# Kernel optimization log

Hardware: AMD Instinct MI355X
Metric: run time of the kernel (lower is better)

The kernel has to match this reference:

```python
import jax, jax.numpy as jnp
import numpy as np

N_ELEM = 10   # len(EnvPara.ELEMENTS)
N_ATOMS = 100000
N_DIM = 256


def setup_inputs() -> dict:
    key = jax.random.key(0)
    k = jax.random.split(key, 5)
    return {
        "input_tensor": jax.random.normal(k[0], (N_ATOMS, N_DIM), jnp.float32),
        "species": jax.random.randint(k[1], (N_ATOMS,), 0, N_ELEM, dtype=jnp.int64),
        "W1": jax.random.normal(k[2], (N_ELEM, N_DIM, N_DIM), jnp.float32) / np.sqrt(N_DIM).astype(np.float32),
        "b1": jnp.zeros((N_ELEM, N_DIM), jnp.float32),
        "W2": jax.random.normal(k[3], (N_ELEM, N_DIM, 1), jnp.float32) / np.sqrt(N_DIM).astype(np.float32),
        "b2": jnp.zeros((N_ELEM, 1), jnp.float32),
    }


def _element_linear(x, species, W, b):
    # Species-routed linear: each atom uses the weight/bias of its element.
    # Loop over the small fixed element set (N_ELEM=10) to avoid materializing
    # a [n_atoms, d_in, d_out] gathered-weight tensor.
    out = jnp.zeros((x.shape[0], W.shape[2]), dtype=x.dtype)
    for e in range(W.shape[0]):
        mask = (species == e)[:, None]                      # [n_atoms, 1]
        out = out + jnp.where(mask, x @ W[e] + b[e], jnp.zeros((), x.dtype))
    return out


def reference(input_tensor, species, W1, b1, W2, b2):
    # layer2(silu(layer1(x)))
    h = _element_linear(input_tensor, species, W1, b1)      # [n_atoms, n_dim]
    h = jax.nn.silu(h)                                      # way=0 -> plain SiLU
    return _element_linear(h, species, W2, b2)              # [n_atoms, 1]
```

## Files before the change

kernel.cpp:

```cpp
#include <hip/hip_runtime.h>
#include <hip/hip_bf16.h>
#include <stdint.h>


#define NDIM 256
#define CHUNKS 16
#define BCHUNK 16384
#define TROWS 32
#define ROWB 1040
#define MAXT 16
#define NB_GEMM 256

typedef __attribute__((ext_vector_type(8))) short short8;
typedef __attribute__((ext_vector_type(8))) unsigned short ushort8;
typedef __attribute__((ext_vector_type(4))) float f32x4;

__device__ __forceinline__ unsigned short f2bf(float f) {
  unsigned u = __float_as_uint(f);
  u = (u + 0x7FFFu + ((u >> 16) & 1u)) >> 16;
  return (unsigned short)u;
}

__device__ __forceinline__ void gload_lds16(const void* gsrc, void* ldst) {
  __builtin_amdgcn_global_load_lds(
      (const __attribute__((address_space(1))) unsigned*)gsrc,
      (__attribute__((address_space(3))) unsigned*)(uintptr_t)(unsigned)(uintptr_t)ldst,
      16, 0, 0);
}

__device__ __forceinline__ short8 cvt8(float4 lo, float4 hi) {
  union { short8 s; unsigned u[4]; } r;
  __hip_bfloat162 t;
  t = __float22bfloat162_rn(make_float2(lo.x, lo.y)); r.u[0] = *(unsigned*)&t;
  t = __float22bfloat162_rn(make_float2(lo.z, lo.w)); r.u[1] = *(unsigned*)&t;
  t = __float22bfloat162_rn(make_float2(hi.x, hi.y)); r.u[2] = *(unsigned*)&t;
  t = __float22bfloat162_rn(make_float2(hi.z, hi.w)); r.u[3] = *(unsigned*)&t;
  return r.s;
}


__global__ void convw_k(const float* __restrict__ W1, unsigned short* __restrict__ wt, int NE) {
  int t = blockIdx.x * 256 + threadIdx.x;
  if (t >= NE * 8192) return;
  int n = t & 255;
  int g = (t >> 8) & 3;
  int step = (t >> 10) & 7;
  int e = t >> 13;
  int k0 = step * 32 + g * 8;
  const float* src = W1 + ((size_t)e << 16) + (size_t)k0 * NDIM + n;
  unsigned short v[8];
  #pragma unroll
  for (int j = 0; j < 8; ++j) v[j] = f2bf(src[j * NDIM]);
  char* chunk = (char*)wt + (size_t)(e * 8 + step) * BCHUNK;
  unsigned off = ((unsigned)(n * 64 + g * 16)) ^ ((unsigned)((n & 7) << 4));
  *(ushort8*)(chunk + off) = *(ushort8*)v;
}

__global__ void bhist_k(const int* __restrict__ sp, int n, int* __restrict__ bc, int NE) {
  __shared__ int wc[4][16];
  int tid = threadIdx.x;
  int i = blockIdx.x * 256 + tid;
  int s = (i < n) ? sp[i] : -1;
  int w = tid >> 6, lane = tid & 63;
  for (int e = 0; e < NE; ++e) {
    unsigned long long m = __ballot(s == e);
    if (lane == 0) wc[w][e] = __popcll(m);
  }
  __syncthreads();
  if (tid < NE) bc[blockIdx.x * NE + tid] = wc[0][tid] + wc[1][tid] + wc[2][tid] + wc[3][tid];
}

__global__ void scan_k(const int* __restrict__ bc, int* __restrict__ bo,
                       int* __restrict__ atom_start, int* __restrict__ tile_off,
                       int* __restrict__ bstart, int nblocks, int NE) {
  __shared__ int csum[256];
  __shared__ int coff[256];
  __shared__ int stot[16];
  __shared__ int sbase[16];
  int tid = threadIdx.x;
  int per = (nblocks + CHUNKS - 1) / CHUNKS;
  int e = tid / CHUNKS, c = tid % CHUNKS;
  int b0 = c * per, b1 = b0 + per; if (b1 > nblocks) b1 = nblocks;
  if (tid < NE * CHUNKS) {
    int s = 0;
    for (int b = b0; b < b1; ++b) s += bc[b * NE + e];
    csum[tid] = s;
  }
  __syncthreads();
  if (tid < NE) {
    int r = 0;
    for (int c2 = 0; c2 < CHUNKS; ++c2) { coff[tid * CHUNKS + c2] = r; r += csum[tid * CHUNKS + c2]; }
    stot[tid] = r;
  }
  __syncthreads();
  if (tid == 0) {
    int a = 0, t = 0;
    for (int e2 = 0; e2 < NE; ++e2) {
      sbase[e2] = a;
      atom_start[e2] = a; tile_off[e2] = t;
      a += stot[e2]; t += (stot[e2] + TROWS - 1) / TROWS;
    }
    atom_start[NE] = a; tile_off[NE] = t;
    int ntl = t > 0 ? t : 1;
    int nbk[16]; int tot = 0, emax = 0;
    for (int e2 = 0; e2 < NE; ++e2) {
      int nt = tile_off[e2 + 1] - tile_off[e2];
      int v = (nt > 0) ? (int)(((long long)nt * NB_GEMM) / ntl) : 0;
      if (nt > 0 && v < 1) v = 1;
      nbk[e2] = v; tot += v;
      if (nbk[e2] > nbk[emax]) emax = e2;
    }
    nbk[emax] += NB_GEMM - tot;
    int bacc = 0;
    for (int e2 = 0; e2 < NE; ++e2) { bstart[e2] = bacc; bacc += nbk[e2]; }
    bstart[NE] = bacc;
  }
  __syncthreads();
  if (tid < NE * CHUNKS) {
    int run = sbase[e] + coff[tid];
    for (int b = b0; b < b1; ++b) { bo[b * NE + e] = run; run += bc[b * NE + e]; }
  }
}

__global__ void dscatter_k(const int* __restrict__ sp, int n, const int* __restrict__ bo,
                           int* __restrict__ sorted, int NE) {
  __shared__ int wc[4][16];
  int tid = threadIdx.x;
  int i = blockIdx.x * 256 + tid;
  int s = (i < n) ? sp[i] : -1;
  int w = tid >> 6, lane = tid & 63;
  for (int e = 0; e < NE; ++e) {
    unsigned long long m = __ballot(s == e);
    if (lane == 0) wc[w][e] = __popcll(m);
  }
  __syncthreads();
  for (int e = 0; e < NE; ++e) {
    unsigned long long m = __ballot(s == e);
    if (s == e) {
      int wpre = 0;
      for (int w2 = 0; w2 < 4; ++w2) if (w2 < w) wpre += wc[w2][e];
      int rank = __popcll(m & ((1ull << lane) - 1ull));
      sorted[bo[blockIdx.x * NE + e] + wpre + rank] = i;
    }
  }
}


__global__ __launch_bounds__(512, 1) void gemm_k(
    const float* __restrict__ x, const unsigned short* __restrict__ wt,
    const float* __restrict__ b1, const float* __restrict__ w2,
    const float* __restrict__ b2, const int* __restrict__ sorted,
    const int* __restrict__ atom_start, const int* __restrict__ tile_off,
    const int* __restrict__ bstart, float* __restrict__ out, int NE)
{
  __shared__ __align__(16) char ldsA[3][TROWS * ROWB];
  __shared__ float partLds[256];
  __shared__ int ldsAtoms[MAXT * TROWS];
  __shared__ int toffs[17], astart[17], bst[17];

  int tid = threadIdx.x, lane = tid & 63, wid = tid >> 6;
  int lr = lane & 15, lg = lane >> 4;

  if (tid <= NE) {
    toffs[tid] = tile_off[tid]; astart[tid] = atom_start[tid]; bst[tid] = bstart[tid];
  }
  __syncthreads();

  int b = blockIdx.x;
  int e = 0;
  while (b >= bst[e + 1]) ++e;
  int j = b - bst[e], nbe = bst[e + 1] - bst[e];
  int nte = toffs[e + 1] - toffs[e];
  int q = nte / nbe, r = nte % nbe;
  int cnt = q + (j < r ? 1 : 0);
  if (cnt <= 0) return;
  int t0 = toffs[e] + j * q + (j < r ? j : r);
  int t1 = t0 + cnt;

  {
    int rs0 = astart[e] + (t0 - toffs[e]) * TROWS;
    int rvAll = astart[e + 1] - rs0;
    for (int i = tid; i < cnt * TROWS; i += 512) {
      int rloc = (i < rvAll) ? i : (rvAll - 1);
      ldsAtoms[i] = sorted[rs0 + rloc];
    }
  }
  __syncthreads();

  short8 bf[2][8];
  float bbv[2], wvv[2];
  {
    const char* wbase = (const char*)wt + (size_t)e * 8 * BCHUNK;
    #pragma unroll
    for (int nf = 0; nf < 2; ++nf) {
      int ncol = wid * 32 + nf * 16 + lr;
      unsigned off = ((unsigned)(ncol * 64 + lg * 16)) ^ ((unsigned)((ncol & 7) << 4));
      #pragma unroll
      for (int s = 0; s < 8; ++s)
        bf[nf][s] = *(const short8*)(wbase + (size_t)s * BCHUNK + off);
      bbv[nf] = b1[(size_t)e * NDIM + ncol];
      wvv[nf] = w2[(size_t)e * NDIM + ncol];
    }
  }
  float b2v = b2[e];
  #pragma unroll
  for (int nf = 0; nf < 2; ++nf)
    #pragma unroll
    for (int s = 0; s < 8; ++s)
      asm volatile("" :: "v"(bf[nf][s]));

  auto stageA = [&](int t, int buf) {
    int base = (t - t0) * TROWS;
    #pragma unroll
    for (int i = 0; i < 4; ++i) {
      int rrow = wid * 4 + i;
      int atom = ldsAtoms[base + rrow];
      gload_lds16(x + (size_t)atom * NDIM + lane * 4, &ldsA[buf][rrow * ROWB]);
    }
  };

  stageA(t0, 0);
  stageA(t0 + 1 < t1 ? t0 + 1 : t1 - 1, 1);

  for (int t = t0; t < t1; ++t) {
    int buf = (t - t0) % 3;

    int ts = t + 2 < t1 ? t + 2 : t1 - 1;
    stageA(ts, (t - t0 + 2) % 3);

    if (t == t0)          { asm volatile("s_waitcnt vmcnt(8)" ::: "memory"); }
    else if (t == t0 + 1) { asm volatile("s_waitcnt vmcnt(9)" ::: "memory"); }
    else                  { asm volatile("s_waitcnt vmcnt(10)" ::: "memory"); }
    __builtin_amdgcn_s_barrier();
    __builtin_amdgcn_sched_barrier(0);

    f32x4 acc[2][2];
    const f32x4 zero = {0.f, 0.f, 0.f, 0.f};
    #pragma unroll
    for (int i = 0; i < 2; ++i)
      #pragma unroll
      for (int jj = 0; jj < 2; ++jj) acc[i][jj] = zero;

    const char* Ab = ldsA[buf];
    #pragma unroll
    for (int step = 0; step < 8; ++step) {
      int k0 = step * 32;
      short8 af[2];
      #pragma unroll
      for (int mf = 0; mf < 2; ++mf) {
        const char* p = Ab + (mf * 16 + lr) * ROWB + (k0 + lg * 8) * 4;
        float4 lo = *(const float4*)p;
        float4 hi = *(const float4*)(p + 16);
        af[mf] = cvt8(lo, hi);
      }
      #pragma unroll
      for (int mf = 0; mf < 2; ++mf)
        #pragma unroll
        for (int nf = 0; nf < 2; ++nf)
          acc[mf][nf] = __builtin_amdgcn_mfma_f32_16x16x32_bf16(af[mf], bf[nf][step], acc[mf][nf], 0, 0, 0);
    }

    float psum[2][4];
    #pragma unroll
    for (int mf = 0; mf < 2; ++mf)
      #pragma unroll
      for (int rg = 0; rg < 4; ++rg) psum[mf][rg] = 0.f;

    #pragma unroll
    for (int nf = 0; nf < 2; ++nf) {
      #pragma unroll
      for (int mf = 0; mf < 2; ++mf)
        #pragma unroll
        for (int rg = 0; rg < 4; ++rg) {
          float h = acc[mf][nf][rg] + bbv[nf];
          float sv = h * __builtin_amdgcn_rcpf(1.f + __expf(-h));
          psum[mf][rg] += sv * wvv[nf];
        }
    }
    #pragma unroll
    for (int mf = 0; mf < 2; ++mf)
      #pragma unroll
      for (int rg = 0; rg < 4; ++rg) {
        float v = psum[mf][rg];
        v += __shfl_xor(v, 1, 64);
        v += __shfl_xor(v, 2, 64);
        v += __shfl_xor(v, 4, 64);
        v += __shfl_xor(v, 8, 64);
        psum[mf][rg] = v;
      }
    if (lr == 0) {
      #pragma unroll
      for (int mf = 0; mf < 2; ++mf)
        #pragma unroll
        for (int rg = 0; rg < 4; ++rg)
          partLds[wid * TROWS + mf * 16 + lg * 4 + rg] = psum[mf][rg];
    }

    asm volatile("s_waitcnt lgkmcnt(0)" ::: "memory");
    __builtin_amdgcn_s_barrier();
    __builtin_amdgcn_sched_barrier(0);

    if (lane < 4) {
      int rloc = wid * 4 + lane;
      float s = b2v;
      #pragma unroll
      for (int w = 0; w < 8; ++w) s += partLds[w * TROWS + rloc];
      out[ldsAtoms[(t - t0) * TROWS + rloc]] = s;
    }
  }
}


extern "C" void kernel_launch(void* const* d_in, const int* in_sizes, int n_in,
                              void* d_out, int out_size, void* d_ws, size_t ws_size,
                              hipStream_t stream) {
  const float* x  = (const float*)d_in[0];
  const int*   sp = (const int*)d_in[1];
  const float* W1 = (const float*)d_in[2];
  const float* b1 = (const float*)d_in[3];
  const float* W2 = (const float*)d_in[4];
  const float* b2 = (const float*)d_in[5];
  float* out = (float*)d_out;

  int n_atoms = in_sizes[0] / NDIM;
  int NE = in_sizes[2] / (NDIM * NDIM);
  int nblocks = (n_atoms + 255) / 256;

  char* wsb = (char*)d_ws;
  size_t o = 0;
  int* bc = (int*)(wsb + o);         o += ((size_t)nblocks * NE * 4 + 255) & ~(size_t)255;
  int* bo = (int*)(wsb + o);         o += ((size_t)nblocks * NE * 4 + 255) & ~(size_t)255;
  int* atom_start = (int*)(wsb + o); o += 256;
  int* tile_off   = (int*)(wsb + o); o += 256;
  int* bstart     = (int*)(wsb + o); o += 256;
  int* sorted     = (int*)(wsb + o); o += ((size_t)n_atoms * 4 + 255) & ~(size_t)255;
  unsigned short* wt = (unsigned short*)(wsb + o);

  hipLaunchKernelGGL(convw_k, dim3((NE * 8192 + 255) / 256), dim3(256), 0, stream,
                     W1, wt, NE);
  hipLaunchKernelGGL(bhist_k, dim3(nblocks), dim3(256), 0, stream, sp, n_atoms, bc, NE);
  hipLaunchKernelGGL(scan_k, dim3(1), dim3(256), 0, stream, bc, bo, atom_start, tile_off,
                     bstart, nblocks, NE);
  hipLaunchKernelGGL(dscatter_k, dim3(nblocks), dim3(256), 0, stream, sp, n_atoms, bo,
                     sorted, NE);

  hipLaunchKernelGGL(gemm_k, dim3(NB_GEMM), dim3(512), 0, stream,
                     x, wt, b1, W2, b2, sorted, atom_start, tile_off, bstart, out, NE);
}
```

Measured before the change: 75.90 us.

## Stage activations through registers as swizzled bf16 in LDS once per tile

Replaces the triple-buffered direct global-to-LDS fp32 staging with register prefetch of the next tile. Each thread converts its fp32 values to bf16 once and writes them into a single XOR-swizzled LDS tile. Previously every wave re-converted fp32 to bf16 on each MFMA step. The change cuts LDS footprint and read bandwidth and removes redundant conversions, and it doubles the GEMM block count. In exchange it keeps only one tile of lookahead in registers and adds a barrier per tile with a single LDS buffer. It also caps tiles per block at MAXT.

```diff
diff --git a/kernel.cpp b/kernel.cpp
--- a/kernel.cpp
+++ b/kernel.cpp
@@ -7,13 +7,13 @@
 #define CHUNKS 16
 #define BCHUNK 16384
 #define TROWS 32
-#define ROWB 1040
 #define MAXT 16
-#define NB_GEMM 256
+#define NB_GEMM 512
 
 typedef __attribute__((ext_vector_type(8))) short short8;
 typedef __attribute__((ext_vector_type(8))) unsigned short ushort8;
 typedef __attribute__((ext_vector_type(4))) float f32x4;
+typedef __attribute__((ext_vector_type(2))) unsigned u32x2;
 
 __device__ __forceinline__ unsigned short f2bf(float f) {
   unsigned u = __float_as_uint(f);
@@ -21,21 +21,8 @@
   return (unsigned short)u;
 }
 
-__device__ __forceinline__ void gload_lds16(const void* gsrc, void* ldst) {
-  __builtin_amdgcn_global_load_lds(
-      (const __attribute__((address_space(1))) unsigned*)gsrc,
-      (__attribute__((address_space(3))) unsigned*)(uintptr_t)(unsigned)(uintptr_t)ldst,
-      16, 0, 0);
-}
-
-__device__ __forceinline__ short8 cvt8(float4 lo, float4 hi) {
-  union { short8 s; unsigned u[4]; } r;
-  __hip_bfloat162 t;
-  t = __float22bfloat162_rn(make_float2(lo.x, lo.y)); r.u[0] = *(unsigned*)&t;
-  t = __float22bfloat162_rn(make_float2(lo.z, lo.w)); r.u[1] = *(unsigned*)&t;
-  t = __float22bfloat162_rn(make_float2(hi.x, hi.y)); r.u[2] = *(unsigned*)&t;
-  t = __float22bfloat162_rn(make_float2(hi.z, hi.w)); r.u[3] = *(unsigned*)&t;
-  return r.s;
+__device__ __forceinline__ unsigned pk2(float a, float b) {
+  return (unsigned)f2bf(a) | ((unsigned)f2bf(b) << 16);
 }
 
 
@@ -153,7 +140,7 @@
     const int* __restrict__ atom_start, const int* __restrict__ tile_off,
     const int* __restrict__ bstart, float* __restrict__ out, int NE)
 {
-  __shared__ __align__(16) char ldsA[3][TROWS * ROWB];
+  __shared__ __align__(16) char ldsT[TROWS * 512];
   __shared__ float partLds[256];
   __shared__ int ldsAtoms[MAXT * TROWS];
   __shared__ int toffs[17], astart[17], bst[17];
@@ -174,6 +161,7 @@
   int q = nte / nbe, r = nte % nbe;
   int cnt = q + (j < r ? 1 : 0);
   if (cnt <= 0) return;
+  if (cnt > MAXT) cnt = MAXT;
   int t0 = toffs[e] + j * q + (j < r ? j : r);
   int t1 = t0 + cnt;
 
@@ -204,33 +192,50 @@
   }
   float b2v = b2[e];
   #pragma unroll
-  for (int nf = 0; nf < 2; ++nf)
-    #pragma unroll
-    for (int s = 0; s < 8; ++s)
-      asm volatile("" :: "v"(bf[nf][s]));
-
-  auto stageA = [&](int t, int buf) {
-    int base = (t - t0) * TROWS;
-    #pragma unroll
-    for (int i = 0; i < 4; ++i) {
-      int rrow = wid * 4 + i;
-      int atom = ldsAtoms[base + rrow];
-      gload_lds16(x + (size_t)atom * NDIM + lane * 4, &ldsA[buf][rrow * ROWB]);
-    }
-  };
-
-  stageA(t0, 0);
-  stageA(t0 + 1 < t1 ? t0 + 1 : t1 - 1, 1);
+  for (int nf = 0; nf < 2; ++nf) {
+    #pragma unroll
+    for (int s = 0; s < 8; ++s) asm volatile("" : "+v"(bf[nf][s]));
+    asm volatile("" : "+v"(bbv[nf]), "+v"(wvv[nf]));
+  }
+
+  int srow = tid >> 4;
+  int skc  = tid & 15;
+  unsigned swzW = (unsigned)((srow & 7) << 4);
+  unsigned rbW  = (unsigned)(srow * 512 + skc * 8);
+  unsigned swzA = (unsigned)((lr & 7) << 4);
+
+  float4 xr0, xr1, xr2, xr3;
+  {
+    int atom = ldsAtoms[srow];
+    const float* xp = x + (size_t)atom * NDIM + skc * 4;
+    xr0 = *(const float4*)(xp);
+    xr1 = *(const float4*)(xp + 64);
+    xr2 = *(const float4*)(xp + 128);
+    xr3 = *(const float4*)(xp + 192);
+  }
 
   for (int t = t0; t < t1; ++t) {
-    int buf = (t - t0) % 3;
-
-    int ts = t + 2 < t1 ? t + 2 : t1 - 1;
-    stageA(ts, (t - t0 + 2) % 3);
-
-    if (t == t0)          { asm volatile("s_waitcnt vmcnt(8)" ::: "memory"); }
-    else if (t == t0 + 1) { asm volatile("s_waitcnt vmcnt(9)" ::: "memory"); }
-    else                  { asm volatile("s_waitcnt vmcnt(10)" ::: "memory"); }
+    {
+      u32x2 w;
+      w[0] = pk2(xr0.x, xr0.y); w[1] = pk2(xr0.z, xr0.w);
+      *(u32x2*)(ldsT + ((rbW +   0) ^ swzW)) = w;
+      w[0] = pk2(xr1.x, xr1.y); w[1] = pk2(xr1.z, xr1.w);
+      *(u32x2*)(ldsT + ((rbW + 128) ^ swzW)) = w;
+      w[0] = pk2(xr2.x, xr2.y); w[1] = pk2(xr2.z, xr2.w);
+      *(u32x2*)(ldsT + ((rbW + 256) ^ swzW)) = w;
+      w[0] = pk2(xr3.x, xr3.y); w[1] = pk2(xr3.z, xr3.w);
+      *(u32x2*)(ldsT + ((rbW + 384) ^ swzW)) = w;
+    }
+    if (t + 1 < t1) {
+      int atom = ldsAtoms[(t + 1 - t0) * TROWS + srow];
+      const float* xp = x + (size_t)atom * NDIM + skc * 4;
+      xr0 = *(const float4*)(xp);
+      xr1 = *(const float4*)(xp + 64);
+      xr2 = *(const float4*)(xp + 128);
+      xr3 = *(const float4*)(xp + 192);
+    }
+
+    asm volatile("s_waitcnt lgkmcnt(0)" ::: "memory");
     __builtin_amdgcn_s_barrier();
     __builtin_amdgcn_sched_barrier(0);
 
@@ -241,17 +246,13 @@
       #pragma unroll
       for (int jj = 0; jj < 2; ++jj) acc[i][jj] = zero;
 
-    const char* Ab = ldsA[buf];
     #pragma unroll
     for (int step = 0; step < 8; ++step) {
-      int k0 = step * 32;
       short8 af[2];
       #pragma unroll
       for (int mf = 0; mf < 2; ++mf) {
-        const char* p = Ab + (mf * 16 + lr) * ROWB + (k0 + lg * 8) * 4;
-        float4 lo = *(const float4*)p;
-        float4 hi = *(const float4*)(p + 16);
-        af[mf] = cvt8(lo, hi);
+        unsigned off = ((unsigned)((mf * 16 + lr) * 512 + step * 64 + lg * 16)) ^ swzA;
+        af[mf] = *(const short8*)(ldsT + off);
       }
       #pragma unroll
       for (int mf = 0; mf < 2; ++mf)
```

After: 69.97 us. -7.8%, faster.
